# Optimization experiments

Hardware: AMD Instinct MI355X
Metric: run time of the kernel (lower is better)

## Reference

```python
import jax, jax.numpy as jnp
import numpy as np

N, D, C = 100000, 384, 8


def setup_inputs() -> dict:
    key = jax.random.key(0)
    k1, k2, k3, k4 = jax.random.split(key, 4)
    Y = jax.random.normal(k1, (N, D), dtype=jnp.float32)
    O = jax.random.bernoulli(k2, 0.9, (N, D))  # observation mask
    # learned VB parameters (as held in the nn.Parameters of VBPCA)
    mbar = 0.1 * jax.random.normal(k3, (D,), dtype=jnp.float32)
    wbar = 0.1 * jax.random.normal(k4, (D, C), dtype=jnp.float32)
    Sigmaw = jnp.broadcast_to(jnp.eye(C, dtype=jnp.float32), (D, C, C))
    vy = jnp.float32(1.0)
    return {"Y": Y, "O": O, "mbar": mbar, "wbar": wbar, "Sigmaw": Sigmaw, "vy": vy}


def reference(Y, O, mbar, wbar, Sigmaw, vy):
    O_ = O.astype(Y.dtype)            # [N, D]
    Y = jnp.nan_to_num(Y)
    # per-channel rank-c outer product plus Sigmaw: baddbmm(Sigmaw, wbar[:,:,None], wbar[:,None,:])
    OwwSw = Sigmaw + wbar[:, :, None] * wbar[:, None, :]            # [D, C, C]
    # accumulate over observed channels: [N, D] @ [D, C*C] -> [N, C, C]
    A = (O_ @ OwwSw.reshape(D, C * C)).reshape(-1, C, C)
    Ic = jnp.eye(C, dtype=Y.dtype)
    Sigma_xn = vy * jnp.linalg.inv(vy * Ic[None] + A)               # [N, C, C]
    # xbarn = einsum('nlk,ni,ik,ni->nl', Sigma_xn/vy, O_, wbar, Y - mbar)
    t = O_ * (Y - mbar)                                             # [N, D]
    proj = t @ wbar                                                 # [N, C]
    xbarn = jnp.einsum('nlk,nk->nl', Sigma_xn / vy, proj)           # [N, C]
    return xbarn, Sigma_xn
```

## Files before the change

### kernel.cpp

```cpp
#include <hip/hip_runtime.h>

#define NN 100000
#define DD 384
#define CC 8
#define ROWS 64
#define WROWS 16
#define CROWS 8
#define TSTR 200

typedef unsigned int uint;
typedef _Float16 half8 __attribute__((ext_vector_type(8)));
typedef float floatx4 __attribute__((ext_vector_type(4)));

__device__ __forceinline__ constexpr int TIDX(int i, int j) { return i * (i + 1) / 2 + j; }

__device__ __forceinline__ uint pkh2(float a, float b) {
  return __builtin_bit_cast(uint, __builtin_amdgcn_cvt_pkrtz(a, b));
}

__global__ __launch_bounds__(64) void vbpca_prep(
    const float* __restrict__ wbar, const float* __restrict__ Sigmaw,
    uint4* __restrict__ bfrag) {
  const int l = threadIdx.x;
  const int kt = blockIdx.x;
  const int kgrp = l >> 4;
#pragma unroll
  for (int ct = 0; ct < 3; ++ct) {
    const int col = ct * 16 + (l & 15);
    int ii = 0;
#pragma unroll
    for (int t = 0; t < 7; ++t) {
      if ((ii + 1) * (ii + 2) / 2 <= col && ii < 7) ++ii;
    }
    const int jj = col - ii * (ii + 1) / 2;
    float v[8];
#pragma unroll
    for (int j = 0; j < 8; ++j) {
      const int d = kt * 32 + kgrp * 8 + j;
      float val;
      if (col < 36) {
        val = Sigmaw[(size_t)d * 64 + ii * 8 + jj] + wbar[d * 8 + ii] * wbar[d * 8 + jj];
      } else if (col < 44) {
        val = wbar[d * 8 + (col - 36)];
      } else {
        val = 0.f;
      }
      v[j] = val;
    }
    uint4 u;
    u.x = pkh2(v[0], v[1]); u.y = pkh2(v[2], v[3]);
    u.z = pkh2(v[4], v[5]); u.w = pkh2(v[6], v[7]);
    bfrag[(kt * 3 + ct) * 64 + l] = u;
  }
}

__global__ __launch_bounds__(256, 3) void vbpca_main(
    const float* __restrict__ Y, const int* __restrict__ O,
    const uint4* __restrict__ bfrag, const float* __restrict__ mbar,
    const float* __restrict__ vyp, float* __restrict__ out) {
  __shared__ uint smem[13184];
  float* mbar_l = (float*)smem;
  uint* tile = smem + 384;
  float* scat_l = (float*)(smem + 384);
  float* sigst = (float*)(smem + 384);
  float* xbst = (float*)(smem + 384) + 4160;

  const int tid = threadIdx.x;
  const int wu = __builtin_amdgcn_readfirstlane((int)(tid >> 6));
  const int l = tid & 63;

  for (int i = tid; i < DD; i += 256) mbar_l[i] = mbar[i];
  __syncthreads();

  uint* wtile = tile + wu * (16 * TSTR);
  const int r0c0 = blockIdx.x * ROWS + wu * WROWS;
  const int r0c1 = r0c0 + CROWS;

  float4 yv[2][3];
  int4 ov[2][3];

#define LOADSTG(B, S, R0)                                                   \
  {                                                                         \
    _Pragma("unroll") for (int j = 0; j < 3; ++j) {                         \
      const int f4 = (S)*192 + j * 64 + l;  \
      const int i = f4 / 96;                                                \
      const int c96 = f4 - i * 96;                                          \
      int row = (R0) + i;                                                   \
      row = row < NN ? row : NN - 1;                                        \
      const size_t off = (size_t)row * 96 + c96;                            \
      yv[B][j] = reinterpret_cast<const float4*>(Y)[off];                   \
      ov[B][j] = reinterpret_cast<const int4*>(O)[off];                     \
    }                                                                       \
  }

#define PACKSTG(B, S)                                                       \
  {                                                                         \
    _Pragma("unroll") for (int j = 0; j < 3; ++j) {                         \
      const int f4 = (S)*192 + j * 64 + l;                                  \
      const int i = f4 / 96;                                                \
      const int c96 = f4 - i * 96;                                          \
      const float4 mb = *reinterpret_cast<const float4*>(mbar_l + c96 * 4); \
      const float4 y = yv[B][j];                                            \
      const int4 o = ov[B][j];                                              \
      const float f0 = (float)o.x, f1 = (float)o.y;                         \
      const float f2 = (float)o.z, f3 = (float)o.w;                         \
      uint* po = wtile + (2 * i) * TSTR + c96 * 2;                          \
      *reinterpret_cast<uint2*>(po) = make_uint2(pkh2(f0, f1), pkh2(f2, f3)); \
      uint* pt = wtile + (2 * i + 1) * TSTR + c96 * 2;                      \
      *reinterpret_cast<uint2*>(pt) =                                       \
          make_uint2(pkh2(f0 * (y.x - mb.x), f1 * (y.y - mb.y)),            \
                     pkh2(f2 * (y.z - mb.z), f3 * (y.w - mb.w)));           \
    }                                                                       \
  }

  floatx4 accA[3], accB[3];
#pragma unroll
  for (int j = 0; j < 3; ++j) {
    accA[j] = (floatx4){0.f, 0.f, 0.f, 0.f};
    accB[j] = (floatx4){0.f, 0.f, 0.f, 0.f};
  }

#define MFMA_LOOP(ACC)                                                      \
  {                                                                         \
    uint4 bf0 = bfrag[0 * 64 + l];                                          \
    uint4 bf1 = bfrag[1 * 64 + l];                                          \
    uint4 bf2 = bfrag[2 * 64 + l];                                          \
    _Pragma("unroll") for (int kt = 0; kt < 12; ++kt) {                     \
      const half8 av = *reinterpret_cast<const half8*>(                     \
          wtile + (l & 15) * TSTR + kt * 16 + (l >> 4) * 4);                \
      uint4 nb0, nb1, nb2;                                                  \
      if (kt < 11) {                                                        \
        nb0 = bfrag[((kt + 1) * 3 + 0) * 64 + l];                           \
        nb1 = bfrag[((kt + 1) * 3 + 1) * 64 + l];                           \
        nb2 = bfrag[((kt + 1) * 3 + 2) * 64 + l];                           \
      }                                                                     \
      ACC[0] = __builtin_amdgcn_mfma_f32_16x16x32_f16(                      \
          av, __builtin_bit_cast(half8, bf0), ACC[0], 0, 0, 0);             \
      ACC[1] = __builtin_amdgcn_mfma_f32_16x16x32_f16(                      \
          av, __builtin_bit_cast(half8, bf1), ACC[1], 0, 0, 0);             \
      ACC[2] = __builtin_amdgcn_mfma_f32_16x16x32_f16(                      \
          av, __builtin_bit_cast(half8, bf2), ACC[2], 0, 0, 0);             \
      bf0 = nb0; bf1 = nb1; bf2 = nb2;                                      \
    }                                                                       \
  }

  LOADSTG(0, 0, r0c0);
  LOADSTG(1, 1, r0c0);
  PACKSTG(0, 0);
  LOADSTG(0, 2, r0c0);
  PACKSTG(1, 1);
  LOADSTG(1, 3, r0c0);
  PACKSTG(0, 2);
  PACKSTG(1, 3);
  LOADSTG(0, 0, r0c1);
  LOADSTG(1, 1, r0c1);
  MFMA_LOOP(accA);

  PACKSTG(0, 0);
  LOADSTG(0, 2, r0c1);
  PACKSTG(1, 1);
  LOADSTG(1, 3, r0c1);
  PACKSTG(0, 2);
  PACKSTG(1, 3);
  MFMA_LOOP(accB);

  __syncthreads();

#pragma unroll
  for (int ct = 0; ct < 3; ++ct) {
#pragma unroll
    for (int reg = 0; reg < 4; ++reg) {
      const int m = (l >> 4) * 4 + reg;
      scat_l[(wu * 32 + m) * 49 + ct * 16 + (l & 15)] = accA[ct][reg];
      scat_l[(wu * 32 + 16 + m) * 49 + ct * 16 + (l & 15)] = accB[ct][reg];
    }
  }
  __syncthreads();

  float a[36], pr[CC];
  if (tid < 64) {
#pragma unroll
    for (int k = 0; k < 36; ++k) a[k] = scat_l[(2 * tid) * 49 + k];
#pragma unroll
    for (int j = 0; j < CC; ++j) pr[j] = scat_l[(2 * tid + 1) * 49 + 36 + j];
  }
  __syncthreads();

  if (tid < 64) {
    const int row = tid;
    const float vy = *vyp;

    float L[36];
#pragma unroll
    for (int j = 0; j < CC; ++j) {
      float s = a[TIDX(j, j)] + vy;
#pragma unroll
      for (int k = 0; k < CC; ++k) {
        if (k < j) s -= L[TIDX(j, k)] * L[TIDX(j, k)];
      }
      const float dj = sqrtf(s);
      L[TIDX(j, j)] = dj;
      const float invdj = 1.0f / dj;
#pragma unroll
      for (int i = j + 1; i < CC; ++i) {
        float tt = a[TIDX(i, j)];
#pragma unroll
        for (int k = 0; k < CC; ++k) {
          if (k < j) tt -= L[TIDX(i, k)] * L[TIDX(j, k)];
        }
        L[TIDX(i, j)] = tt * invdj;
      }
    }

    float invd[CC];
#pragma unroll
    for (int i = 0; i < CC; ++i) invd[i] = 1.0f / L[TIDX(i, i)];
    float Li[36];
#pragma unroll
    for (int j = 0; j < CC; ++j) {
      Li[TIDX(j, j)] = invd[j];
#pragma unroll
      for (int i = j + 1; i < CC; ++i) {
        float s = 0.f;
#pragma unroll
        for (int k = 0; k < CC; ++k) {
          if (k >= j && k < i) s += L[TIDX(i, k)] * Li[TIDX(k, j)];
        }
        Li[TIDX(i, j)] = -s * invd[i];
      }
    }

    float sig[36];
#pragma unroll
    for (int i = 0; i < CC; ++i) {
#pragma unroll
      for (int j = 0; j <= i; ++j) {
        float s = 0.f;
#pragma unroll
        for (int k = 0; k < CC; ++k) {
          if (k >= i) s += Li[TIDX(k, i)] * Li[TIDX(k, j)];
        }
        sig[TIDX(i, j)] = vy * s;
      }
    }

    float uvec[CC];
#pragma unroll
    for (int i = 0; i < CC; ++i) {
      float s = 0.f;
#pragma unroll
      for (int j = 0; j < CC; ++j) {
        if (j <= i) s += Li[TIDX(i, j)] * pr[j];
      }
      uvec[i] = s;
    }
#pragma unroll
    for (int ll = 0; ll < CC; ++ll) {
      float s = 0.f;
#pragma unroll
      for (int i = 0; i < CC; ++i) {
        if (i >= ll) s += Li[TIDX(i, ll)] * uvec[i];
      }
      xbst[row * 9 + ll] = s;
    }
#pragma unroll
    for (int i = 0; i < CC; ++i) {
#pragma unroll
      for (int j = 0; j < CC; ++j) {
        sigst[row * 65 + i * 8 + j] = (j <= i) ? sig[TIDX(i, j)] : sig[TIDX(j, i)];
      }
    }
  }
  __syncthreads();

  const int valid = (NN - blockIdx.x * ROWS < ROWS) ? (NN - blockIdx.x * ROWS) : ROWS;
  float* __restrict__ sig_out = out + (size_t)NN * CC + (size_t)blockIdx.x * ROWS * 64;
  for (int f = tid; f < valid * 64; f += 256) {
    sig_out[f] = sigst[(f >> 6) * 65 + (f & 63)];
  }
  float* __restrict__ xb_out = out + (size_t)blockIdx.x * ROWS * CC;
  for (int f = tid; f < valid * 8; f += 256) {
    xb_out[f] = xbst[(f >> 3) * 9 + (f & 7)];
  }
}

extern "C" void kernel_launch(void* const* d_in, const int* in_sizes, int n_in,
                              void* d_out, int out_size, void* d_ws, size_t ws_size,
                              hipStream_t stream) {
  const float* Y = (const float*)d_in[0];
  const int* O = (const int*)d_in[1];
  const float* mbar = (const float*)d_in[2];
  const float* wbar = (const float*)d_in[3];
  const float* Sigmaw = (const float*)d_in[4];
  const float* vyp = (const float*)d_in[5];
  float* out = (float*)d_out;
  uint4* bfrag = (uint4*)d_ws;

  vbpca_prep<<<12, 64, 0, stream>>>(wbar, Sigmaw, bfrag);
  vbpca_main<<<(NN + ROWS - 1) / ROWS, 256, 0, stream>>>(Y, O, bfrag, mbar, vyp, out);
}
```

Measured before the change: 82.36 us.

## Restructure per-chunk pipeline with 3-deep bfrag prefetch and sched barriers

Replaces the 1-deep B-fragment prefetch with a 3-stage register ring that is preloaded during packing, so global loads of bfrag run further ahead of the MFMAs. The second chunk's global loads no longer overlap the first chunk's MFMA loop, and scheduling barriers separate the chunks. The LDS row stride is reduced from 200 to 196, shrinking shared memory and changing the bank mapping. This adds register pressure from nine live uint4 fragments and loses some cross-chunk load/compute overlap.

```diff
diff --git a/kernel.cpp b/kernel.cpp
--- a/kernel.cpp
+++ b/kernel.cpp
@@ -6,7 +6,7 @@
 #define ROWS 64
 #define WROWS 16
 #define CROWS 8
-#define TSTR 200
+#define TSTR 196
 
 typedef unsigned int uint;
 typedef _Float16 half8 __attribute__((ext_vector_type(8)));
@@ -58,7 +58,7 @@
     const float* __restrict__ Y, const int* __restrict__ O,
     const uint4* __restrict__ bfrag, const float* __restrict__ mbar,
     const float* __restrict__ vyp, float* __restrict__ out) {
-  __shared__ uint smem[13184];
+  __shared__ uint smem[12928];
   float* mbar_l = (float*)smem;
   uint* tile = smem + 384;
   float* scat_l = (float*)(smem + 384);
@@ -78,11 +78,12 @@
 
   float4 yv[2][3];
   int4 ov[2][3];
+  uint4 bfr[3][3];
 
 #define LOADSTG(B, S, R0)                                                   \
   {                                                                         \
     _Pragma("unroll") for (int j = 0; j < 3; ++j) {                         \
-      const int f4 = (S)*192 + j * 64 + l;  \
+      const int f4 = (S)*192 + j * 64 + l;                                  \
       const int i = f4 / 96;                                                \
       const int c96 = f4 - i * 96;                                          \
       int row = (R0) + i;                                                   \
@@ -120,49 +121,43 @@
     accB[j] = (floatx4){0.f, 0.f, 0.f, 0.f};
   }
 
-#define MFMA_LOOP(ACC)                                                      \
+#define DO_CHUNK(R0, ACC)                                                   \
   {                                                                         \
-    uint4 bf0 = bfrag[0 * 64 + l];                                          \
-    uint4 bf1 = bfrag[1 * 64 + l];                                          \
-    uint4 bf2 = bfrag[2 * 64 + l];                                          \
+    LOADSTG(0, 0, R0);                                                      \
+    LOADSTG(1, 1, R0);                                                      \
+    PACKSTG(0, 0);                                                          \
+    LOADSTG(0, 2, R0);                                                      \
+    PACKSTG(1, 1);                                                          \
+    LOADSTG(1, 3, R0);                                                      \
+    _Pragma("unroll") for (int d = 0; d < 3; ++d) {                         \
+      _Pragma("unroll") for (int c = 0; c < 3; ++c) {                       \
+        bfr[d][c] = bfrag[(d * 3 + c) * 64 + l];                            \
+      }                                                                     \
+    }                                                                       \
+    PACKSTG(0, 2);                                                          \
+    PACKSTG(1, 3);                                                          \
     _Pragma("unroll") for (int kt = 0; kt < 12; ++kt) {                     \
+      const int s = kt % 3;                                                 \
       const half8 av = *reinterpret_cast<const half8*>(                     \
           wtile + (l & 15) * TSTR + kt * 16 + (l >> 4) * 4);                \
-      uint4 nb0, nb1, nb2;                                                  \
-      if (kt < 11) {                                                        \
-        nb0 = bfrag[((kt + 1) * 3 + 0) * 64 + l];                           \
-        nb1 = bfrag[((kt + 1) * 3 + 1) * 64 + l];                           \
-        nb2 = bfrag[((kt + 1) * 3 + 2) * 64 + l];                           \
+      ACC[0] = __builtin_amdgcn_mfma_f32_16x16x32_f16(                      \
+          av, __builtin_bit_cast(half8, bfr[s][0]), ACC[0], 0, 0, 0);       \
+      ACC[1] = __builtin_amdgcn_mfma_f32_16x16x32_f16(                      \
+          av, __builtin_bit_cast(half8, bfr[s][1]), ACC[1], 0, 0, 0);       \
+      ACC[2] = __builtin_amdgcn_mfma_f32_16x16x32_f16(                      \
+          av, __builtin_bit_cast(half8, bfr[s][2]), ACC[2], 0, 0, 0);       \
+      if (kt + 3 < 12) {                                                    \
+        _Pragma("unroll") for (int c = 0; c < 3; ++c) {                     \
+          bfr[s][c] = bfrag[((kt + 3) * 3 + c) * 64 + l];                   \
+        }                                                                   \
       }                                                                     \
-      ACC[0] = __builtin_amdgcn_mfma_f32_16x16x32_f16(                      \
-          av, __builtin_bit_cast(half8, bf0), ACC[0], 0, 0, 0);             \
-      ACC[1] = __builtin_amdgcn_mfma_f32_16x16x32_f16(                      \
-          av, __builtin_bit_cast(half8, bf1), ACC[1], 0, 0, 0);             \
-      ACC[2] = __builtin_amdgcn_mfma_f32_16x16x32_f16(                      \
-          av, __builtin_bit_cast(half8, bf2), ACC[2], 0, 0, 0);             \
-      bf0 = nb0; bf1 = nb1; bf2 = nb2;                                      \
-    }                                                                       \
-  }
-
-  LOADSTG(0, 0, r0c0);
-  LOADSTG(1, 1, r0c0);
-  PACKSTG(0, 0);
-  LOADSTG(0, 2, r0c0);
-  PACKSTG(1, 1);
-  LOADSTG(1, 3, r0c0);
-  PACKSTG(0, 2);
-  PACKSTG(1, 3);
-  LOADSTG(0, 0, r0c1);
-  LOADSTG(1, 1, r0c1);
-  MFMA_LOOP(accA);
-
-  PACKSTG(0, 0);
-  LOADSTG(0, 2, r0c1);
-  PACKSTG(1, 1);
-  LOADSTG(1, 3, r0c1);
-  PACKSTG(0, 2);
-  PACKSTG(1, 3);
-  MFMA_LOOP(accB);
+    }                                                                       \
+  }
+
+  DO_CHUNK(r0c0, accA);
+  __builtin_amdgcn_sched_barrier(0);
+  DO_CHUNK(r0c1, accB);
+  __builtin_amdgcn_sched_barrier(0);
 
   __syncthreads();
 
```

After: 89.55 us. +8.7%, slower.

## Halve LDS tile by splitting K into two halves and interleaving MFMA with staging

Applied to the files above, without the earlier changes.

Each wave's LDS staging tile now holds only half of the D dimension (192 channels), and the MFMA accumulation is split into two half-K passes interleaved with loading and packing of the next stage. This halves shared memory per block, and the launch bounds are raised to request 4 blocks per CU instead of 3. Loads are reorganised so each stage covers a column chunk across all 8 rows rather than contiguous rows. The aim is higher occupancy and better overlap of global loads with MFMA work. The cost is more register pressure under the tighter bound and less coalesced per-row access.

```diff
diff --git a/kernel.cpp b/kernel.cpp
--- a/kernel.cpp
+++ b/kernel.cpp
@@ -6,7 +6,7 @@
 #define ROWS 64
 #define WROWS 16
 #define CROWS 8
-#define TSTR 200
+#define TSTR 100
 
 typedef unsigned int uint;
 typedef _Float16 half8 __attribute__((ext_vector_type(8)));
@@ -54,11 +54,11 @@
   }
 }
 
-__global__ __launch_bounds__(256, 3) void vbpca_main(
+__global__ __launch_bounds__(256, 4) void vbpca_main(
     const float* __restrict__ Y, const int* __restrict__ O,
     const uint4* __restrict__ bfrag, const float* __restrict__ mbar,
     const float* __restrict__ vyp, float* __restrict__ out) {
-  __shared__ uint smem[13184];
+  __shared__ uint smem[6784];
   float* mbar_l = (float*)smem;
   uint* tile = smem + 384;
   float* scat_l = (float*)(smem + 384);
@@ -82,12 +82,12 @@
 #define LOADSTG(B, S, R0)                                                   \
   {                                                                         \
     _Pragma("unroll") for (int j = 0; j < 3; ++j) {                         \
-      const int f4 = (S)*192 + j * 64 + l;  \
-      const int i = f4 / 96;                                                \
-      const int c96 = f4 - i * 96;                                          \
+      const int f = j * 64 + l;                                             \
+      const int i = f / 24;                                                 \
+      const int c = f - i * 24;                                             \
       int row = (R0) + i;                                                   \
       row = row < NN ? row : NN - 1;                                        \
-      const size_t off = (size_t)row * 96 + c96;                            \
+      const size_t off = (size_t)row * 96 + (S)*24 + c;                     \
       yv[B][j] = reinterpret_cast<const float4*>(Y)[off];                   \
       ov[B][j] = reinterpret_cast<const int4*>(O)[off];                     \
     }                                                                       \
@@ -96,17 +96,19 @@
 #define PACKSTG(B, S)                                                       \
   {                                                                         \
     _Pragma("unroll") for (int j = 0; j < 3; ++j) {                         \
-      const int f4 = (S)*192 + j * 64 + l;                                  \
-      const int i = f4 / 96;                                                \
-      const int c96 = f4 - i * 96;                                          \
-      const float4 mb = *reinterpret_cast<const float4*>(mbar_l + c96 * 4); \
+      const int f = j * 64 + l;                                             \
+      const int i = f / 24;                                                 \
+      const int c = f - i * 24;                                             \
+      const float4 mb =                                                     \
+          *reinterpret_cast<const float4*>(mbar_l + ((S)*24 + c) * 4);      \
       const float4 y = yv[B][j];                                            \
       const int4 o = ov[B][j];                                              \
       const float f0 = (float)o.x, f1 = (float)o.y;                         \
       const float f2 = (float)o.z, f3 = (float)o.w;                         \
-      uint* po = wtile + (2 * i) * TSTR + c96 * 2;                          \
+      const int lc = (((S)&1) * 24 + c) * 2;                                \
+      uint* po = wtile + (2 * i) * TSTR + lc;                               \
       *reinterpret_cast<uint2*>(po) = make_uint2(pkh2(f0, f1), pkh2(f2, f3)); \
-      uint* pt = wtile + (2 * i + 1) * TSTR + c96 * 2;                      \
+      uint* pt = wtile + (2 * i + 1) * TSTR + lc;                           \
       *reinterpret_cast<uint2*>(pt) =                                       \
           make_uint2(pkh2(f0 * (y.x - mb.x), f1 * (y.y - mb.y)),            \
                      pkh2(f2 * (y.z - mb.z), f3 * (y.w - mb.w)));           \
@@ -120,19 +122,19 @@
     accB[j] = (floatx4){0.f, 0.f, 0.f, 0.f};
   }
 
-#define MFMA_LOOP(ACC)                                                      \
+#define MFMA_HALF(ACC, H)                                                   \
   {                                                                         \
-    uint4 bf0 = bfrag[0 * 64 + l];                                          \
-    uint4 bf1 = bfrag[1 * 64 + l];                                          \
-    uint4 bf2 = bfrag[2 * 64 + l];                                          \
-    _Pragma("unroll") for (int kt = 0; kt < 12; ++kt) {                     \
+    uint4 bf0 = bfrag[(((H)*6 + 0) * 3 + 0) * 64 + l];                      \
+    uint4 bf1 = bfrag[(((H)*6 + 0) * 3 + 1) * 64 + l];                      \
+    uint4 bf2 = bfrag[(((H)*6 + 0) * 3 + 2) * 64 + l];                      \
+    _Pragma("unroll") for (int ktl = 0; ktl < 6; ++ktl) {                   \
       const half8 av = *reinterpret_cast<const half8*>(                     \
-          wtile + (l & 15) * TSTR + kt * 16 + (l >> 4) * 4);                \
+          wtile + (l & 15) * TSTR + ktl * 16 + (l >> 4) * 4);               \
       uint4 nb0, nb1, nb2;                                                  \
-      if (kt < 11) {                                                        \
-        nb0 = bfrag[((kt + 1) * 3 + 0) * 64 + l];                           \
-        nb1 = bfrag[((kt + 1) * 3 + 1) * 64 + l];                           \
-        nb2 = bfrag[((kt + 1) * 3 + 2) * 64 + l];                           \
+      if (ktl < 5) {                                                        \
+        nb0 = bfrag[(((H)*6 + ktl + 1) * 3 + 0) * 64 + l];                  \
+        nb1 = bfrag[(((H)*6 + ktl + 1) * 3 + 1) * 64 + l];                  \
+        nb2 = bfrag[(((H)*6 + ktl + 1) * 3 + 2) * 64 + l];                  \
       }                                                                     \
       ACC[0] = __builtin_amdgcn_mfma_f32_16x16x32_f16(                      \
           av, __builtin_bit_cast(half8, bf0), ACC[0], 0, 0, 0);             \
@@ -150,19 +152,20 @@
   LOADSTG(0, 2, r0c0);
   PACKSTG(1, 1);
   LOADSTG(1, 3, r0c0);
+  MFMA_HALF(accA, 0);
   PACKSTG(0, 2);
+  LOADSTG(0, 0, r0c1);
   PACKSTG(1, 3);
-  LOADSTG(0, 0, r0c1);
   LOADSTG(1, 1, r0c1);
-  MFMA_LOOP(accA);
-
+  MFMA_HALF(accA, 1);
   PACKSTG(0, 0);
   LOADSTG(0, 2, r0c1);
   PACKSTG(1, 1);
   LOADSTG(1, 3, r0c1);
+  MFMA_HALF(accB, 0);
   PACKSTG(0, 2);
   PACKSTG(1, 3);
-  MFMA_LOOP(accB);
+  MFMA_HALF(accB, 1);
 
   __syncthreads();
 
```

New measurement: 94.41 us. 14.6% more time.

## Gather MFMA A-fragments directly from global memory, dropping LDS staging tile

Applied to the files above, without the earlier changes.

Each lane now loads its own Y/O slice from global memory, applies the mask and mean subtraction, and packs the half8 A-fragment in registers, instead of staging packed rows through a shared-memory tile. Lane parity selects whether the fragment holds the mask row or the masked residual row. This shrinks LDS use and raises the occupancy hint from 3 to 4 blocks per CU. The cost is less coalesced global access: each lane reads 32-byte chunks at a row stride, and neighbouring lane pairs load the same data twice. The explicit software prefetch of the next stage is also gone.

```diff
diff --git a/kernel.cpp b/kernel.cpp
--- a/kernel.cpp
+++ b/kernel.cpp
@@ -4,9 +4,6 @@
 #define DD 384
 #define CC 8
 #define ROWS 64
-#define WROWS 16
-#define CROWS 8
-#define TSTR 200
 
 typedef unsigned int uint;
 typedef _Float16 half8 __attribute__((ext_vector_type(8)));
@@ -54,16 +51,15 @@
   }
 }
 
-__global__ __launch_bounds__(256, 3) void vbpca_main(
+__global__ __launch_bounds__(256, 4) void vbpca_main(
     const float* __restrict__ Y, const int* __restrict__ O,
     const uint4* __restrict__ bfrag, const float* __restrict__ mbar,
     const float* __restrict__ vyp, float* __restrict__ out) {
-  __shared__ uint smem[13184];
-  float* mbar_l = (float*)smem;
-  uint* tile = smem + 384;
-  float* scat_l = (float*)(smem + 384);
-  float* sigst = (float*)(smem + 384);
-  float* xbst = (float*)(smem + 384) + 4160;
+  __shared__ float smemf[6656];
+  float* mbar_l = smemf;
+  float* scat_l = smemf + 384;
+  float* sigst = smemf + 384;
+  float* xbst = smemf + 384 + 4160;
 
   const int tid = threadIdx.x;
   const int wu = __builtin_amdgcn_readfirstlane((int)(tid >> 6));
@@ -72,46 +68,19 @@
   for (int i = tid; i < DD; i += 256) mbar_l[i] = mbar[i];
   __syncthreads();
 
-  uint* wtile = tile + wu * (16 * TSTR);
-  const int r0c0 = blockIdx.x * ROWS + wu * WROWS;
-  const int r0c1 = r0c0 + CROWS;
-
-  float4 yv[2][3];
-  int4 ov[2][3];
-
-#define LOADSTG(B, S, R0)                                                   \
-  {                                                                         \
-    _Pragma("unroll") for (int j = 0; j < 3; ++j) {                         \
-      const int f4 = (S)*192 + j * 64 + l;  \
-      const int i = f4 / 96;                                                \
-      const int c96 = f4 - i * 96;                                          \
-      int row = (R0) + i;                                                   \
-      row = row < NN ? row : NN - 1;                                        \
-      const size_t off = (size_t)row * 96 + c96;                            \
-      yv[B][j] = reinterpret_cast<const float4*>(Y)[off];                   \
-      ov[B][j] = reinterpret_cast<const int4*>(O)[off];                     \
-    }                                                                       \
-  }
-
-#define PACKSTG(B, S)                                                       \
-  {                                                                         \
-    _Pragma("unroll") for (int j = 0; j < 3; ++j) {                         \
-      const int f4 = (S)*192 + j * 64 + l;                                  \
-      const int i = f4 / 96;                                                \
-      const int c96 = f4 - i * 96;                                          \
-      const float4 mb = *reinterpret_cast<const float4*>(mbar_l + c96 * 4); \
-      const float4 y = yv[B][j];                                            \
-      const int4 o = ov[B][j];                                              \
-      const float f0 = (float)o.x, f1 = (float)o.y;                         \
-      const float f2 = (float)o.z, f3 = (float)o.w;                         \
-      uint* po = wtile + (2 * i) * TSTR + c96 * 2;                          \
-      *reinterpret_cast<uint2*>(po) = make_uint2(pkh2(f0, f1), pkh2(f2, f3)); \
-      uint* pt = wtile + (2 * i + 1) * TSTR + c96 * 2;                      \
-      *reinterpret_cast<uint2*>(pt) =                                       \
-          make_uint2(pkh2(f0 * (y.x - mb.x), f1 * (y.y - mb.y)),            \
-                     pkh2(f2 * (y.z - mb.z), f3 * (y.w - mb.w)));           \
-    }                                                                       \
-  }
+  const int rt0 = blockIdx.x * ROWS + wu * 16;
+  int gr0 = rt0 + ((l & 15) >> 1);
+  gr0 = gr0 < NN ? gr0 : NN - 1;
+  int gr1 = rt0 + 8 + ((l & 15) >> 1);
+  gr1 = gr1 < NN ? gr1 : NN - 1;
+  const float tsel = (float)(l & 1);
+  const float osel = 1.f - tsel;
+  const int kgo = (l >> 4) * 8;
+
+  const float* __restrict__ Yr0 = Y + (size_t)gr0 * DD;
+  const int* __restrict__ Or0 = O + (size_t)gr0 * DD;
+  const float* __restrict__ Yr1 = Y + (size_t)gr1 * DD;
+  const int* __restrict__ Or1 = O + (size_t)gr1 * DD;
 
   floatx4 accA[3], accB[3];
 #pragma unroll
@@ -120,14 +89,37 @@
     accB[j] = (floatx4){0.f, 0.f, 0.f, 0.f};
   }
 
-#define MFMA_LOOP(ACC)                                                      \
+#define GATHER_FRAG(YR, OR, KT, FRAG)                                       \
+  {                                                                         \
+    const int kb = (KT) * 32 + kgo;                                         \
+    const float4 ylo = *reinterpret_cast<const float4*>((YR) + kb);         \
+    const float4 yhi = *reinterpret_cast<const float4*>((YR) + kb + 4);     \
+    const int4 olo = *reinterpret_cast<const int4*>((OR) + kb);             \
+    const int4 ohi = *reinterpret_cast<const int4*>((OR) + kb + 4);         \
+    const float4 mlo = *reinterpret_cast<const float4*>(mbar_l + kb);       \
+    const float4 mhi = *reinterpret_cast<const float4*>(mbar_l + kb + 4);   \
+    const float v0 = (float)olo.x * fmaf(tsel, ylo.x - mlo.x, osel);        \
+    const float v1 = (float)olo.y * fmaf(tsel, ylo.y - mlo.y, osel);        \
+    const float v2 = (float)olo.z * fmaf(tsel, ylo.z - mlo.z, osel);        \
+    const float v3 = (float)olo.w * fmaf(tsel, ylo.w - mlo.w, osel);        \
+    const float v4 = (float)ohi.x * fmaf(tsel, yhi.x - mhi.x, osel);        \
+    const float v5 = (float)ohi.y * fmaf(tsel, yhi.y - mhi.y, osel);        \
+    const float v6 = (float)ohi.z * fmaf(tsel, yhi.z - mhi.z, osel);        \
+    const float v7 = (float)ohi.w * fmaf(tsel, yhi.w - mhi.w, osel);        \
+    uint4 fu;                                                               \
+    fu.x = pkh2(v0, v1); fu.y = pkh2(v2, v3);                               \
+    fu.z = pkh2(v4, v5); fu.w = pkh2(v6, v7);                               \
+    FRAG = __builtin_bit_cast(half8, fu);                                   \
+  }
+
+#define MTILE_LOOP(YR, OR, ACC)                                             \
   {                                                                         \
     uint4 bf0 = bfrag[0 * 64 + l];                                          \
     uint4 bf1 = bfrag[1 * 64 + l];                                          \
     uint4 bf2 = bfrag[2 * 64 + l];                                          \
     _Pragma("unroll") for (int kt = 0; kt < 12; ++kt) {                     \
-      const half8 av = *reinterpret_cast<const half8*>(                     \
-          wtile + (l & 15) * TSTR + kt * 16 + (l >> 4) * 4);                \
+      half8 av;                                                             \
+      GATHER_FRAG(YR, OR, kt, av);                                          \
       uint4 nb0, nb1, nb2;                                                  \
       if (kt < 11) {                                                        \
         nb0 = bfrag[((kt + 1) * 3 + 0) * 64 + l];                           \
@@ -144,25 +136,8 @@
     }                                                                       \
   }
 
-  LOADSTG(0, 0, r0c0);
-  LOADSTG(1, 1, r0c0);
-  PACKSTG(0, 0);
-  LOADSTG(0, 2, r0c0);
-  PACKSTG(1, 1);
-  LOADSTG(1, 3, r0c0);
-  PACKSTG(0, 2);
-  PACKSTG(1, 3);
-  LOADSTG(0, 0, r0c1);
-  LOADSTG(1, 1, r0c1);
-  MFMA_LOOP(accA);
-
-  PACKSTG(0, 0);
-  LOADSTG(0, 2, r0c1);
-  PACKSTG(1, 1);
-  LOADSTG(1, 3, r0c1);
-  PACKSTG(0, 2);
-  PACKSTG(1, 3);
-  MFMA_LOOP(accB);
+  MTILE_LOOP(Yr0, Or0, accA);
+  MTILE_LOOP(Yr1, Or1, accB);
 
   __syncthreads();
 
```

New measurement: 89.89 us. +9.1%, slower.
